# Kernel optimization log

Measured on AMD Instinct MI355X. Metric: run time of the kernel, lower is better.

Reference implementation:

```python
import jax, jax.numpy as jnp
import numpy as np

H = 128          # hidden_dim
N_LAYERS = 3
N_GRAPHS = 256
LN_EPS = 1e-5


def setup_inputs() -> dict:
    key = jax.random.key(0)
    ks = jax.random.split(key, 12)
    N, E = 100000, 600000
    x = jax.random.normal(ks[0], (N, 66), dtype=jnp.float32)
    edge_index = jax.random.randint(ks[1], (2, E), 0, N, dtype=jnp.int32)
    edge_attr = jax.random.normal(ks[2], (E, 6), dtype=jnp.float32)
    batch = jnp.sort(jax.random.randint(ks[3], (N,), 0, N_GRAPHS, dtype=jnp.int32))
    # params (stored as [in, out] so y = x @ W + b)
    def lin(k, fan_in, fan_out):
        s = 1.0 / np.sqrt(fan_in)
        kw, kb = jax.random.split(k)
        return (jax.random.uniform(kw, (fan_in, fan_out), jnp.float32, -s, s),
                jax.random.uniform(kb, (fan_out,), jnp.float32, -s, s))
    w_node, b_node = lin(ks[4], 66, H)
    w_edge, b_edge = lin(ks[5], 6, H)
    mp_ws, mp_bs = [], []
    for i in range(N_LAYERS):
        w, b = lin(ks[6 + i], 3 * H, H)
        mp_ws.append(w); mp_bs.append(b)
    w_out, b_out = lin(ks[9], H, H)
    return {
        "x": x, "edge_index": edge_index, "edge_attr": edge_attr, "batch": batch,
        "w_node": w_node, "b_node": b_node, "w_edge": w_edge, "b_edge": b_edge,
        "mp_w": jnp.stack(mp_ws), "mp_b": jnp.stack(mp_bs),
        "ln_g": jnp.ones((H,), jnp.float32), "ln_b": jnp.zeros((H,), jnp.float32),
        "w_out": w_out, "b_out": b_out,
    }


def _layer_norm(h, g, b):
    mu = h.mean(-1, keepdims=True)
    var = ((h - mu) ** 2).mean(-1, keepdims=True)
    return (h - mu) * jax.lax.rsqrt(var + LN_EPS) * g + b


def reference(x, edge_index, edge_attr, batch, w_node, b_node, w_edge, b_edge,
              mp_w, mp_b, ln_g, ln_b, w_out, b_out):
    h = x @ w_node + b_node                      # [N, H]
    ef = edge_attr @ w_edge + b_edge             # [E, H]
    src, dst = edge_index[0], edge_index[1]
    for i in range(N_LAYERS):
        W = mp_w[i]                               # [3H, H], split to avoid concat
        Ws, Wd, We = W[:H], W[H:2 * H], W[2 * H:]
        # per-edge message = Linear(concat(h[src], h[dst], ef)); original takes a
        # GLOBAL mean over all edges -> single [H] vector broadcast to all nodes
        msgs = h[src] @ Ws + h[dst] @ Wd + ef @ We   # [E, H]
        mean_msg = msgs.mean(axis=0) + mp_b[i]       # [H]
        h = h + mean_msg
        h = jax.nn.relu(_layer_norm(h, ln_g, ln_b))
        # dropout is identity in eval mode
    counts = jax.ops.segment_sum(jnp.ones((h.shape[0],), h.dtype), batch,
                                 num_segments=N_GRAPHS)
    pooled = jax.ops.segment_sum(h, batch, num_segments=N_GRAPHS)
    pooled = pooled / jnp.maximum(counts, 1.0)[:, None]   # global_mean_pool
    return pooled @ w_out + b_out                 # [N_GRAPHS, H]
```

## Files before the change

### kernel.cpp

```cpp
#include <hip/hip_runtime.h>

#define HDIM 128
#define XDIM 66
#define EDIM 6
#define NGRAPHS 256
#define LN_EPS 1e-5f

#define HBINS 25600
#define HR 4
#define HB 16
#define CBINS (HR * HBINS)
#define NBX 1024
#define KP 104

typedef __attribute__((ext_vector_type(8))) short sv8;
typedef __attribute__((ext_vector_type(4))) float fv4;

__device__ __forceinline__ unsigned short f2bf(float f) {
    unsigned u = __float_as_uint(f);
    return (unsigned short)((u + 0x7FFFu + ((u >> 16) & 1u)) >> 16);
}
__device__ __forceinline__ float bf2f(unsigned short u) {
    return __uint_as_float((unsigned)u << 16);
}

__global__ __launch_bounds__(256) void k_pre(const int* __restrict__ ei,
        float* __restrict__ part, int E, const float* __restrict__ ea,
        float* __restrict__ sum_attr, const float* __restrict__ w_node,
        unsigned short* __restrict__ wtg) {
    __shared__ float lh[HBINS];
    int b = blockIdx.x;
    int t = threadIdx.x;
    if (b < 2 * HR * HB) {
        int s = b & (HB - 1);
        int r = (b / HB) & (HR - 1);
        int a = b / (HB * HR);
        for (int i = t; i < HBINS; i += 256) lh[i] = 0.f;
        __syncthreads();
        const int* src = ei + (size_t)a * E;
        int chunk = (((E + HB - 1) / HB) + 3) & ~3;
        int lo = s * chunk;
        int hi = min(E, lo + chunk);
        int base = r * HBINS;
        if ((E & 3) == 0) {
            for (int i = lo + t * 4; i < hi; i += 256 * 4) {
                if (i + 4 <= hi) {
                    int4 v = *(const int4*)(src + i);
                    unsigned u0 = (unsigned)(v.x - base);
                    unsigned u1 = (unsigned)(v.y - base);
                    unsigned u2 = (unsigned)(v.z - base);
                    unsigned u3 = (unsigned)(v.w - base);
                    if (u0 < HBINS) atomicAdd(&lh[u0], 1.0f);
                    if (u1 < HBINS) atomicAdd(&lh[u1], 1.0f);
                    if (u2 < HBINS) atomicAdd(&lh[u2], 1.0f);
                    if (u3 < HBINS) atomicAdd(&lh[u3], 1.0f);
                } else {
                    for (int j = i; j < hi; ++j) {
                        unsigned u = (unsigned)(src[j] - base);
                        if (u < HBINS) atomicAdd(&lh[u], 1.0f);
                    }
                }
            }
        } else {
            for (int i = lo + t; i < hi; i += 256) {
                unsigned u = (unsigned)(src[i] - base);
                if (u < HBINS) atomicAdd(&lh[u], 1.0f);
            }
        }
        __syncthreads();
        float* dst = part + (size_t)b * HBINS;
        for (int i = t; i < HBINS / 4; i += 256)
            ((float4*)dst)[i] = ((const float4*)lh)[i];
    } else if (b < 2 * HR * HB + 64) {
        int b2 = b - 2 * HR * HB;
        int nchunk = E >> 1;
        float a0 = 0, a1 = 0, a2 = 0, a3 = 0, a4 = 0, a5 = 0;
        for (int c = b2 * 256 + t; c < nchunk; c += 64 * 256) {
            const float4* p = (const float4*)(ea + (size_t)c * 12);
            float4 v0 = p[0], v1 = p[1], v2 = p[2];
            a0 += v0.x + v1.z;  a1 += v0.y + v1.w;  a2 += v0.z + v2.x;
            a3 += v0.w + v2.y;  a4 += v1.x + v2.z;  a5 += v1.y + v2.w;
        }
#pragma unroll
        for (int m = 32; m; m >>= 1) {
            a0 += __shfl_xor(a0, m); a1 += __shfl_xor(a1, m); a2 += __shfl_xor(a2, m);
            a3 += __shfl_xor(a3, m); a4 += __shfl_xor(a4, m); a5 += __shfl_xor(a5, m);
        }
        float (*sb)[6] = (float(*)[6])lh;
        int lane = t & 63, w = t >> 6;
        if (lane == 0) {
            sb[w][0] = a0; sb[w][1] = a1; sb[w][2] = a2;
            sb[w][3] = a3; sb[w][4] = a4; sb[w][5] = a5;
        }
        __syncthreads();
        if (t < 6) {
            float s = sb[0][t] + sb[1][t] + sb[2][t] + sb[3][t];
            atomicAdd(&sum_attr[t], s);
        }
        if (b2 == 0 && t < 6 && (E & 1))
            atomicAdd(&sum_attr[t], ea[(size_t)(E - 1) * 6 + t]);
    } else {
        if (t < 128) {
            for (int kp = 0; kp < KP; ++kp) {
                float v = (kp < XDIM) ? w_node[kp * HDIM + t] : 0.f;
                wtg[t * KP + kp] = f2bf(v);
            }
        }
    }
}

__global__ __launch_bounds__(256) void k_hist_red(const float* __restrict__ part,
        float* __restrict__ c_src, float* __restrict__ c_dst) {
    int n = blockIdx.x * 256 + threadIdx.x;
    if (n >= CBINS) return;
    int r = n / HBINS, off = n - r * HBINS;
    const float* p0 = part + ((size_t)(0 * HR + r) * HB) * HBINS + off;
    const float* p1 = part + ((size_t)(1 * HR + r) * HB) * HBINS + off;
    float s0 = 0.f, s1 = 0.f;
#pragma unroll 8
    for (int s = 0; s < HB; ++s) {
        s0 += p0[(size_t)s * HBINS];
        s1 += p1[(size_t)s * HBINS];
    }
    c_src[n] = s0;
    c_dst[n] = s1;
}

__global__ __launch_bounds__(256) void k_xsum(const float* __restrict__ x,
        const float* __restrict__ c_src, const float* __restrict__ c_dst,
        float* __restrict__ xpart, int N) {
    int lane = threadIdx.x & 63, w = threadIdx.x >> 6;
    int wid = blockIdx.x * 4 + w, nw = gridDim.x * 4;
    float as0 = 0, ad0 = 0, as1 = 0, ad1 = 0;
    int Q = N >> 2;
    for (int q = wid; q < Q; q += nw) {
        int n = q * 4;
        const float* xr = x + (size_t)n * XDIM;
        float x0 = xr[lane];
        float x1 = xr[XDIM + lane];
        float x2 = xr[2 * XDIM + lane];
        float x3 = xr[3 * XDIM + lane];
        float4 cs = *(const float4*)(c_src + n);
        float4 cd = *(const float4*)(c_dst + n);
        as0 = fmaf(cs.x, x0, as0); as0 = fmaf(cs.y, x1, as0);
        as0 = fmaf(cs.z, x2, as0); as0 = fmaf(cs.w, x3, as0);
        ad0 = fmaf(cd.x, x0, ad0); ad0 = fmaf(cd.y, x1, ad0);
        ad0 = fmaf(cd.z, x2, ad0); ad0 = fmaf(cd.w, x3, ad0);
        if (lane < 2) {
            float e0 = xr[64 + lane];
            float e1 = xr[XDIM + 64 + lane];
            float e2 = xr[2 * XDIM + 64 + lane];
            float e3 = xr[3 * XDIM + 64 + lane];
            as1 = fmaf(cs.x, e0, as1); as1 = fmaf(cs.y, e1, as1);
            as1 = fmaf(cs.z, e2, as1); as1 = fmaf(cs.w, e3, as1);
            ad1 = fmaf(cd.x, e0, ad1); ad1 = fmaf(cd.y, e1, ad1);
            ad1 = fmaf(cd.z, e2, ad1); ad1 = fmaf(cd.w, e3, ad1);
        }
    }
    if (wid == 0) {
        for (int n = Q * 4; n < N; ++n) {
            const float* xr = x + (size_t)n * XDIM;
            float cs = c_src[n], cd = c_dst[n];
            float xv = xr[lane];
            as0 = fmaf(cs, xv, as0);
            ad0 = fmaf(cd, xv, ad0);
            if (lane < 2) {
                float xe = xr[64 + lane];
                as1 = fmaf(cs, xe, as1);
                ad1 = fmaf(cd, xe, ad1);
            }
        }
    }
    __shared__ float redS[4][XDIM], redD[4][XDIM];
    redS[w][lane] = as0;  redD[w][lane] = ad0;
    if (lane < 2) { redS[w][64 + lane] = as1;  redD[w][64 + lane] = ad1; }
    __syncthreads();
    int t = threadIdx.x;
    float* xp = xpart + (size_t)blockIdx.x * 136;
    if (t < XDIM) {
        xp[t]        = redS[0][t] + redS[1][t] + redS[2][t] + redS[3][t];
        xp[XDIM + t] = redD[0][t] + redD[1][t] + redD[2][t] + redD[3][t];
    }
}

__global__ __launch_bounds__(64) void k_xred(const float* __restrict__ xpart,
                                             float* __restrict__ xs, int nb) {
    int e = blockIdx.x;
    int lane = threadIdx.x;
    float s = 0.f;
    for (int b = lane; b < nb; b += 64)
        s += xpart[(size_t)b * 136 + e];
#pragma unroll
    for (int m = 32; m; m >>= 1) s += __shfl_xor(s, m);
    if (lane == 0) xs[e] = s;
}

__global__ __launch_bounds__(256) void k_red(const float* __restrict__ partials,
                                             float* __restrict__ sbuf, int nb) {
    int b0 = blockIdx.x * 32;
    int b1 = min(nb, b0 + 32);
    int t = threadIdx.x;
    float s0 = 0.f, s1 = 0.f;
    for (int b = b0; b < b1; ++b) {
        const float* row = partials + (size_t)b * 512;
        s0 += row[t];
        s1 += row[t + 256];
    }
    atomicAdd(&sbuf[t], s0);
    atomicAdd(&sbuf[t + 256], s1);
}

template <int FIRST>
__global__ __launch_bounds__(256) void k_mm(const float* __restrict__ sv,
        const float* __restrict__ sum_attr, const float* __restrict__ w_edge,
        const float* __restrict__ b_edge, const float* __restrict__ W,
        const float* __restrict__ mpb, float* __restrict__ mean_msg, float Ef,
        const float* __restrict__ w_node, const float* __restrict__ b_node) {
    __shared__ float sc[384];
    __shared__ float mred[256];
    int t = threadIdx.x;
    if (t < 128) {
        float ssrc, sdst;
        if (FIRST) {
            ssrc = Ef * b_node[t];
            sdst = ssrc;
#pragma unroll
            for (int k = 0; k < XDIM; ++k) {
                float wv = w_node[k * HDIM + t];
                ssrc = fmaf(sv[k], wv, ssrc);
                sdst = fmaf(sv[XDIM + k], wv, sdst);
            }
        } else {
            ssrc = sv[t] + sv[t + 128];
            sdst = sv[256 + t] + sv[384 + t];
        }
        sc[t] = ssrc;
        sc[128 + t] = sdst;
        float se = Ef * b_edge[t];
#pragma unroll
        for (int k = 0; k < EDIM; ++k) se = fmaf(sum_attr[k], w_edge[k * HDIM + t], se);
        sc[256 + t] = se;
    }
    __syncthreads();
    int col = blockIdx.x * 16 + (t & 15);
    int rg = t >> 4;
    float acc = 0.f;
#pragma unroll 4
    for (int r = rg * 24; r < rg * 24 + 24; ++r)
        acc = fmaf(sc[r], W[r * HDIM + col], acc);
    mred[t] = acc;
    __syncthreads();
    if (t < 16) {
        float s = 0.f;
#pragma unroll
        for (int g = 0; g < 16; ++g) s += mred[g * 16 + t];
        mean_msg[blockIdx.x * 16 + t] = s / Ef + mpb[blockIdx.x * 16 + t];
    }
}

__global__ __launch_bounds__(256) void k_upd0(
        const float* __restrict__ x, const unsigned short* __restrict__ wtg,
        const float* __restrict__ b_node, const float* __restrict__ mean_msg,
        const float* __restrict__ ln_g, const float* __restrict__ ln_b,
        const float* __restrict__ c_src, const float* __restrict__ c_dst,
        unsigned short* __restrict__ h, float* __restrict__ partials, int N) {
    __shared__ unsigned short xl[64 * KP];
    __shared__ unsigned short wt[128 * KP];
    int t = threadIdx.x;
    int lane = t & 63, w = t >> 6;
    {
        const uint4* srcp = (const uint4*)wtg;
        uint4* dstp = (uint4*)wt;
        for (int i = t; i < 128 * KP / 8; i += 256) dstp[i] = srcp[i];
    }
    for (int i = t; i < 64 * KP / 2; i += 256) ((unsigned*)xl)[i] = 0u;
    __syncthreads();
    int rowbase = blockIdx.x * 64;
    const float* xg = x + (size_t)rowbase * XDIM;
    int lim = min(64, N - rowbase) * XDIM;
    for (int i = t; i < 64 * XDIM; i += 256) {
        if (i < lim) {
            int r = i / XDIM, k = i - r * XDIM;
            xl[r * KP + k] = f2bf(xg[i]);
        }
    }
    int cl = lane & 15, g = lane >> 4;
    float bm[8], gg[8], lb[8];
#pragma unroll
    for (int ct = 0; ct < 8; ++ct) {
        int col = ct * 16 + cl;
        bm[ct] = b_node[col] + mean_msg[col];
        gg[ct] = ln_g[col];
        lb[ct] = ln_b[col];
    }
    __syncthreads();

    fv4 acc[8];
#pragma unroll
    for (int ct = 0; ct < 8; ++ct) acc[ct] = (fv4){0.f, 0.f, 0.f, 0.f};
#pragma unroll
    for (int ks = 0; ks < 3; ++ks) {
        sv8 a = *(const sv8*)&xl[(w * 16 + cl) * KP + ks * 32 + g * 8];
#pragma unroll
        for (int ct = 0; ct < 8; ++ct) {
            sv8 b = *(const sv8*)&wt[(ct * 16 + cl) * KP + ks * 32 + g * 8];
            acc[ct] = __builtin_amdgcn_mfma_f32_16x16x32_bf16(a, b, acc[ct], 0, 0, 0);
        }
    }
    float v[8][4];
    float s[4] = {0.f, 0.f, 0.f, 0.f};
#pragma unroll
    for (int ct = 0; ct < 8; ++ct)
#pragma unroll
        for (int e = 0; e < 4; ++e) {
            v[ct][e] = acc[ct][e] + bm[ct];
            s[e] += v[ct][e];
        }
#pragma unroll
    for (int m = 1; m < 16; m <<= 1) {
        s[0] += __shfl_xor(s[0], m); s[1] += __shfl_xor(s[1], m);
        s[2] += __shfl_xor(s[2], m); s[3] += __shfl_xor(s[3], m);
    }
    float mu[4], q[4] = {0.f, 0.f, 0.f, 0.f};
#pragma unroll
    for (int e = 0; e < 4; ++e) mu[e] = s[e] * (1.0f / HDIM);
#pragma unroll
    for (int ct = 0; ct < 8; ++ct)
#pragma unroll
        for (int e = 0; e < 4; ++e) {
            float d = v[ct][e] - mu[e];
            q[e] = fmaf(d, d, q[e]);
        }
#pragma unroll
    for (int m = 1; m < 16; m <<= 1) {
        q[0] += __shfl_xor(q[0], m); q[1] += __shfl_xor(q[1], m);
        q[2] += __shfl_xor(q[2], m); q[3] += __shfl_xor(q[3], m);
    }
    float rs[4];
#pragma unroll
    for (int e = 0; e < 4; ++e) rs[e] = rsqrtf(q[e] * (1.0f / HDIM) + LN_EPS);

    int grow = rowbase + w * 16 + g * 4;
    float4 csv = *(const float4*)(c_src + grow);
    float4 cdv = *(const float4*)(c_dst + grow);
    float cs[4] = {csv.x, csv.y, csv.z, csv.w};
    float cd[4] = {cdv.x, cdv.y, cdv.z, cdv.w};
    float accS[8], accD[8];
#pragma unroll
    for (int ct = 0; ct < 8; ++ct) { accS[ct] = 0.f; accD[ct] = 0.f; }
#pragma unroll
    for (int e = 0; e < 4; ++e) {
        int row = grow + e;
        bool ok = (row < N);
#pragma unroll
        for (int ct = 0; ct < 8; ++ct) {
            float o = fmaxf(0.f, fmaf((v[ct][e] - mu[e]) * rs[e], gg[ct], lb[ct]));
            if (ok) h[(size_t)row * HDIM + ct * 16 + cl] = f2bf(o);
            accS[ct] = fmaf(cs[e], o, accS[ct]);
            accD[ct] = fmaf(cd[e], o, accD[ct]);
        }
    }
#pragma unroll
    for (int ct = 0; ct < 8; ++ct) {
        accS[ct] += __shfl_xor(accS[ct], 16); accS[ct] += __shfl_xor(accS[ct], 32);
        accD[ct] += __shfl_xor(accD[ct], 16); accD[ct] += __shfl_xor(accD[ct], 32);
    }
    __syncthreads();
    float* redS = (float*)xl;
    float* redD = redS + 512;
    if (g == 0) {
#pragma unroll
        for (int ct = 0; ct < 8; ++ct) {
            redS[w * HDIM + ct * 16 + cl] = accS[ct];
            redD[w * HDIM + ct * 16 + cl] = accD[ct];
        }
    }
    __syncthreads();
    if (t < 128) {
        float ss = redS[t] + redS[128 + t] + redS[256 + t] + redS[384 + t];
        float dd = redD[t] + redD[128 + t] + redD[256 + t] + redD[384 + t];
        float* row = partials + (size_t)blockIdx.x * 512;
        row[t] = ss;       row[t + 128] = 0.f;
        row[t + 256] = dd; row[t + 384] = 0.f;
    }
}

__device__ __forceinline__ float4 ln_row4(const unsigned short* hp,
        float4 mm, float4 g, float4 bb) {
    ushort4 hv = *(const ushort4*)hp;
    float4 v;
    v.x = bf2f(hv.x) + mm.x; v.y = bf2f(hv.y) + mm.y;
    v.z = bf2f(hv.z) + mm.z; v.w = bf2f(hv.w) + mm.w;
    float s = v.x + v.y + v.z + v.w;
#pragma unroll
    for (int m = 1; m < 32; m <<= 1) s += __shfl_xor(s, m);
    float mu = s * (1.0f / HDIM);
    float d0 = v.x - mu, d1 = v.y - mu, d2 = v.z - mu, d3 = v.w - mu;
    float q = d0 * d0 + d1 * d1 + d2 * d2 + d3 * d3;
#pragma unroll
    for (int m = 1; m < 32; m <<= 1) q += __shfl_xor(q, m);
    float rs = rsqrtf(q * (1.0f / HDIM) + LN_EPS);
    float4 o;
    o.x = fmaxf(0.f, fmaf(d0 * rs, g.x, bb.x));
    o.y = fmaxf(0.f, fmaf(d1 * rs, g.y, bb.y));
    o.z = fmaxf(0.f, fmaf(d2 * rs, g.z, bb.z));
    o.w = fmaxf(0.f, fmaf(d3 * rs, g.w, bb.w));
    return o;
}

template <int LAST>
__global__ __launch_bounds__(256) void k_update(
        unsigned short* __restrict__ h, const float* __restrict__ mean_msg,
        const float* __restrict__ ln_g, const float* __restrict__ ln_b,
        const float* __restrict__ c_src, const float* __restrict__ c_dst,
        const int* __restrict__ batch, float* __restrict__ partials,
        float* __restrict__ pooled, int N, int cpb) {
    int t = threadIdx.x;
    int lane = t & 63, w = t >> 6;
    int half = lane >> 5, cl = lane & 31;
    int c0 = cl * 4;
    float4 mm = *(const float4*)(mean_msg + c0);
    float4 g  = *(const float4*)(ln_g + c0);
    float4 bb = *(const float4*)(ln_b + c0);
    int start = blockIdx.x * cpb;
    int end = min(N, start + cpb);
    int spw = (cpb + 3) >> 2;
    int ns = start + w * spw;
    int ne = min(end, ns + spw);
    float4 accS = {0,0,0,0}, accD = {0,0,0,0}, accP = {0,0,0,0};
    int cur_g = -1;
    int n = ns;
    for (; n + 4 <= ne; n += 4) {
        int rA = n + half, rB = n + 2 + half;
        float4 oA = ln_row4(h + (size_t)rA * HDIM + c0, mm, g, bb);
        float4 oB = ln_row4(h + (size_t)rB * HDIM + c0, mm, g, bb);
        if (LAST) {
            int gA = batch[rA], gB = batch[rB];
            if (gA != cur_g) {
                if (cur_g >= 0) {
                    atomicAdd(&pooled[cur_g * HDIM + c0],     accP.x);
                    atomicAdd(&pooled[cur_g * HDIM + c0 + 1], accP.y);
                    atomicAdd(&pooled[cur_g * HDIM + c0 + 2], accP.z);
                    atomicAdd(&pooled[cur_g * HDIM + c0 + 3], accP.w);
                }
                accP = (float4){0,0,0,0};
                cur_g = gA;
            }
            accP.x += oA.x; accP.y += oA.y; accP.z += oA.z; accP.w += oA.w;
            if (gB != cur_g) {
                if (cur_g >= 0) {
                    atomicAdd(&pooled[cur_g * HDIM + c0],     accP.x);
                    atomicAdd(&pooled[cur_g * HDIM + c0 + 1], accP.y);
                    atomicAdd(&pooled[cur_g * HDIM + c0 + 2], accP.z);
                    atomicAdd(&pooled[cur_g * HDIM + c0 + 3], accP.w);
                }
                accP = (float4){0,0,0,0};
                cur_g = gB;
            }
            accP.x += oB.x; accP.y += oB.y; accP.z += oB.z; accP.w += oB.w;
        } else {
            ushort4 pA = {f2bf(oA.x), f2bf(oA.y), f2bf(oA.z), f2bf(oA.w)};
            ushort4 pB = {f2bf(oB.x), f2bf(oB.y), f2bf(oB.z), f2bf(oB.w)};
            *(ushort4*)(h + (size_t)rA * HDIM + c0) = pA;
            *(ushort4*)(h + (size_t)rB * HDIM + c0) = pB;
            float csA = c_src[rA], cdA = c_dst[rA];
            float csB = c_src[rB], cdB = c_dst[rB];
            accS.x = fmaf(csA, oA.x, accS.x); accS.y = fmaf(csA, oA.y, accS.y);
            accS.z = fmaf(csA, oA.z, accS.z); accS.w = fmaf(csA, oA.w, accS.w);
            accS.x = fmaf(csB, oB.x, accS.x); accS.y = fmaf(csB, oB.y, accS.y);
            accS.z = fmaf(csB, oB.z, accS.z); accS.w = fmaf(csB, oB.w, accS.w);
            accD.x = fmaf(cdA, oA.x, accD.x); accD.y = fmaf(cdA, oA.y, accD.y);
            accD.z = fmaf(cdA, oA.z, accD.z); accD.w = fmaf(cdA, oA.w, accD.w);
            accD.x = fmaf(cdB, oB.x, accD.x); accD.y = fmaf(cdB, oB.y, accD.y);
            accD.z = fmaf(cdB, oB.z, accD.z); accD.w = fmaf(cdB, oB.w, accD.w);
        }
    }
    for (; n < ne; n += 2) {
        int row = n + half;
        bool ok = row < ne;
        int rsafe = ok ? row : (N - 1);
        float4 o = ln_row4(h + (size_t)rsafe * HDIM + c0, mm, g, bb);
        if (LAST) {
            if (ok) {
                int gg2 = batch[row];
                if (gg2 != cur_g) {
                    if (cur_g >= 0) {
                        atomicAdd(&pooled[cur_g * HDIM + c0],     accP.x);
                        atomicAdd(&pooled[cur_g * HDIM + c0 + 1], accP.y);
                        atomicAdd(&pooled[cur_g * HDIM + c0 + 2], accP.z);
                        atomicAdd(&pooled[cur_g * HDIM + c0 + 3], accP.w);
                    }
                    accP = (float4){0,0,0,0};
                    cur_g = gg2;
                }
                accP.x += o.x; accP.y += o.y; accP.z += o.z; accP.w += o.w;
            }
        } else if (ok) {
            ushort4 pk = {f2bf(o.x), f2bf(o.y), f2bf(o.z), f2bf(o.w)};
            *(ushort4*)(h + (size_t)row * HDIM + c0) = pk;
            float cs = c_src[row], cd = c_dst[row];
            accS.x = fmaf(cs, o.x, accS.x); accS.y = fmaf(cs, o.y, accS.y);
            accS.z = fmaf(cs, o.z, accS.z); accS.w = fmaf(cs, o.w, accS.w);
            accD.x = fmaf(cd, o.x, accD.x); accD.y = fmaf(cd, o.y, accD.y);
            accD.z = fmaf(cd, o.z, accD.z); accD.w = fmaf(cd, o.w, accD.w);
        }
    }
    if (LAST) {
        if (cur_g >= 0) {
            atomicAdd(&pooled[cur_g * HDIM + c0],     accP.x);
            atomicAdd(&pooled[cur_g * HDIM + c0 + 1], accP.y);
            atomicAdd(&pooled[cur_g * HDIM + c0 + 2], accP.z);
            atomicAdd(&pooled[cur_g * HDIM + c0 + 3], accP.w);
        }
    } else {
        __shared__ float redS[8][HDIM], redD[8][HDIM];
        int set = (w << 1) | half;
        *(float4*)(&redS[set][c0]) = accS;
        *(float4*)(&redD[set][c0]) = accD;
        __syncthreads();
        if (t < 128) {
            float ss = 0.f, dd = 0.f;
#pragma unroll
            for (int gi = 0; gi < 8; ++gi) {
                ss += redS[gi][t];
                dd += redD[gi][t];
            }
            float* row = partials + (size_t)blockIdx.x * 512;
            row[t] = ss;       row[t + 128] = 0.f;
            row[t + 256] = dd; row[t + 384] = 0.f;
        }
    }
}

__global__ __launch_bounds__(128) void k_out(const float* __restrict__ pooled,
        const int* __restrict__ batch, const float* __restrict__ w_out,
        const float* __restrict__ b_out, float* __restrict__ out, int N) {
    int gph = blockIdx.x;
    int t = threadIdx.x;
    __shared__ float p[HDIM];
    __shared__ int cntS;
    if (t == 0) {
        int lo = 0, hi = N;
        while (lo < hi) { int mid = (lo + hi) >> 1; if (batch[mid] < gph) lo = mid + 1; else hi = mid; }
        int lo2 = lo, hi2 = N;
        while (lo2 < hi2) { int mid = (lo2 + hi2) >> 1; if (batch[mid] <= gph) lo2 = mid + 1; else hi2 = mid; }
        cntS = lo2 - lo;
    }
    __syncthreads();
    float inv = 1.0f / fmaxf((float)cntS, 1.0f);
    p[t] = pooled[gph * HDIM + t] * inv;
    __syncthreads();
    float acc = b_out[t];
#pragma unroll 8
    for (int k = 0; k < HDIM; ++k) acc = fmaf(p[k], w_out[k * HDIM + t], acc);
    out[gph * HDIM + t] = acc;
}

extern "C" void kernel_launch(void* const* d_in, const int* in_sizes, int n_in,
                              void* d_out, int out_size, void* d_ws, size_t ws_size,
                              hipStream_t stream) {
    const float* x      = (const float*)d_in[0];
    const int*   ei     = (const int*)d_in[1];
    const float* ea     = (const float*)d_in[2];
    const int*   batch  = (const int*)d_in[3];
    const float* w_node = (const float*)d_in[4];
    const float* b_node = (const float*)d_in[5];
    const float* w_edge = (const float*)d_in[6];
    const float* b_edge = (const float*)d_in[7];
    const float* mp_w   = (const float*)d_in[8];
    const float* mp_b   = (const float*)d_in[9];
    const float* ln_g   = (const float*)d_in[10];
    const float* ln_b   = (const float*)d_in[11];
    const float* w_out  = (const float*)d_in[12];
    const float* b_out  = (const float*)d_in[13];
    float* out = (float*)d_out;
    int N = in_sizes[3];
    int E = in_sizes[2] / EDIM;
    float Ef = (float)E;
    int ntiles0 = (N + 63) / 64;

    float* ws = (float*)d_ws;
    size_t off = 0;
    unsigned short* h = (unsigned short*)(ws + off);
    float* hist_part = ws + off;
    off += (size_t)N * HDIM / 2;
    float* partials = ws + off; off += (size_t)2048 * 512;
    float* mean_msg = ws + off; off += 128;
    float* c_src    = ws + off; off += CBINS;
    float* c_dst    = ws + off; off += CBINS;
    float* xpart    = ws + off; off += (size_t)NBX * 136;
    unsigned short* wtg = (unsigned short*)(ws + off); off += 128 * KP / 2;
    float* xs       = ws + off; off += 136;
    float* acc0     = ws + off;
    float* sum_attr = ws + off; off += 8;
    float* sbuf1    = ws + off; off += 512;
    float* sbuf2    = ws + off; off += 512;
    float* pooled   = ws + off; off += NGRAPHS * HDIM;
    size_t zero_count = (size_t)(ws + off - acc0);
    hipMemsetAsync(acc0, 0, zero_count * sizeof(float), stream);

    k_pre<<<2 * HR * HB + 64 + 1, 256, 0, stream>>>(ei, hist_part, E, ea,
                                                    sum_attr, w_node, wtg);
    k_hist_red<<<(CBINS + 255) / 256, 256, 0, stream>>>(hist_part, c_src, c_dst);
    k_xsum<<<NBX, 256, 0, stream>>>(x, c_src, c_dst, xpart, N);
    k_xred<<<2 * XDIM, 64, 0, stream>>>(xpart, xs, NBX);

    const int NB = 1024;
    int cpb = (N + NB - 1) / NB;

    k_mm<1><<<8, 256, 0, stream>>>(xs, sum_attr, w_edge, b_edge,
                                   mp_w, mp_b, mean_msg, Ef, w_node, b_node);
    k_upd0<<<ntiles0, 256, 0, stream>>>(x, wtg, b_node, mean_msg, ln_g, ln_b,
                                        c_src, c_dst, h, partials, N);
    k_red<<<(ntiles0 + 31) / 32, 256, 0, stream>>>(partials, sbuf1, ntiles0);
    k_mm<0><<<8, 256, 0, stream>>>(sbuf1, sum_attr, w_edge, b_edge,
                                   mp_w + (size_t)1 * 384 * HDIM,
                                   mp_b + (size_t)1 * HDIM, mean_msg, Ef,
                                   w_node, b_node);
    k_update<0><<<NB, 256, 0, stream>>>(h, mean_msg, ln_g, ln_b, c_src, c_dst,
                                        batch, partials, pooled, N, cpb);
    k_red<<<NB / 32, 256, 0, stream>>>(partials, sbuf2, NB);
    k_mm<0><<<8, 256, 0, stream>>>(sbuf2, sum_attr, w_edge, b_edge,
                                   mp_w + (size_t)2 * 384 * HDIM,
                                   mp_b + (size_t)2 * HDIM, mean_msg, Ef,
                                   w_node, b_node);
    k_update<1><<<NB, 256, 0, stream>>>(h, mean_msg, ln_g, ln_b, c_src, c_dst,
                                        batch, partials, pooled, N, cpb);

    k_out<<<NGRAPHS, HDIM, 0, stream>>>(pooled, batch, w_out, b_out, out, N);
}
```

Measured before the change: 163.9 us.

## Byte-pack node degree histogram so one block covers all nodes in LDS

Replaces the range-partitioned float LDS histogram with integer words that pack four 8-bit node counters each, so a single 1024-thread block holds bins for every node. Each edge is now scanned once instead of once per node range, and float atomics become integer atomics. The per-slice partials are reduced with integer adds and unpacked to floats. The edge-attribute sum and weight conversion move into a separate small kernel, which adds a launch. Counts are only correct while every node's in- and out-degree stays below 256, so high-degree graphs would silently give wrong results.

```diff
diff --git a/kernel.cpp b/kernel.cpp
--- a/kernel.cpp
+++ b/kernel.cpp
@@ -6,12 +6,12 @@
 #define NGRAPHS 256
 #define LN_EPS 1e-5f
 
-#define HBINS 25600
-#define HR 4
-#define HB 16
-#define CBINS (HR * HBINS)
+#define NWORDS 25600
+#define CBINS 102400
+#define HB 64
 #define NBX 1024
 #define KP 104
+#define NES 16
 
 typedef __attribute__((ext_vector_type(8))) short sv8;
 typedef __attribute__((ext_vector_type(4))) float fv4;
@@ -24,58 +24,69 @@
     return __uint_as_float((unsigned)u << 16);
 }
 
-__global__ __launch_bounds__(256) void k_pre(const int* __restrict__ ei,
-        float* __restrict__ part, int E, const float* __restrict__ ea,
-        float* __restrict__ sum_attr, const float* __restrict__ w_node,
+__global__ __launch_bounds__(1024) void k_hist(const int* __restrict__ ei,
+        unsigned* __restrict__ part, int E) {
+    __shared__ unsigned lh[NWORDS];
+    int b = blockIdx.x;
+    int s = b & (HB - 1);
+    int a = b / HB;
+    int t = threadIdx.x;
+    for (int i = t; i < NWORDS; i += 1024) lh[i] = 0u;
+    __syncthreads();
+    const int* src = ei + (size_t)a * E;
+    int chunk = (((E + HB - 1) / HB) + 3) & ~3;
+    int lo = s * chunk;
+    int hi = min(E, lo + chunk);
+    if ((E & 3) == 0) {
+        for (int i = lo + t * 4; i + 4 <= hi; i += 1024 * 4) {
+            int4 v = *(const int4*)(src + i);
+            atomicAdd(&lh[v.x >> 2], 1u << ((v.x & 3) * 8));
+            atomicAdd(&lh[v.y >> 2], 1u << ((v.y & 3) * 8));
+            atomicAdd(&lh[v.z >> 2], 1u << ((v.z & 3) * 8));
+            atomicAdd(&lh[v.w >> 2], 1u << ((v.w & 3) * 8));
+        }
+    } else {
+        for (int i = lo + t; i < hi; i += 1024) {
+            int v = src[i];
+            atomicAdd(&lh[v >> 2], 1u << ((v & 3) * 8));
+        }
+    }
+    __syncthreads();
+    unsigned* dst = part + (size_t)b * NWORDS;
+    for (int i = t; i < NWORDS / 4; i += 1024)
+        ((uint4*)dst)[i] = ((const uint4*)lh)[i];
+}
+
+__global__ __launch_bounds__(256) void k_hist_red(const unsigned* __restrict__ part,
+        float* __restrict__ c_src, float* __restrict__ c_dst) {
+    int w = blockIdx.x * 256 + threadIdx.x;
+    if (w >= NWORDS) return;
+    unsigned a0 = 0, a1 = 0;
+    const unsigned* p0 = part + w;
+    const unsigned* p1 = part + (size_t)HB * NWORDS + w;
+#pragma unroll 8
+    for (int s = 0; s < HB; ++s) {
+        a0 += p0[(size_t)s * NWORDS];
+        a1 += p1[(size_t)s * NWORDS];
+    }
+    float4 o0, o1;
+    o0.x = (float)(a0 & 0xFF);         o0.y = (float)((a0 >> 8) & 0xFF);
+    o0.z = (float)((a0 >> 16) & 0xFF); o0.w = (float)(a0 >> 24);
+    o1.x = (float)(a1 & 0xFF);         o1.y = (float)((a1 >> 8) & 0xFF);
+    o1.z = (float)((a1 >> 16) & 0xFF); o1.w = (float)(a1 >> 24);
+    *(float4*)(c_src + 4 * w) = o0;
+    *(float4*)(c_dst + 4 * w) = o1;
+}
+
+__global__ __launch_bounds__(256) void k_misc(const float* __restrict__ ea,
+        float* __restrict__ sum_attr, int E, const float* __restrict__ w_node,
         unsigned short* __restrict__ wtg) {
-    __shared__ float lh[HBINS];
     int b = blockIdx.x;
     int t = threadIdx.x;
-    if (b < 2 * HR * HB) {
-        int s = b & (HB - 1);
-        int r = (b / HB) & (HR - 1);
-        int a = b / (HB * HR);
-        for (int i = t; i < HBINS; i += 256) lh[i] = 0.f;
-        __syncthreads();
-        const int* src = ei + (size_t)a * E;
-        int chunk = (((E + HB - 1) / HB) + 3) & ~3;
-        int lo = s * chunk;
-        int hi = min(E, lo + chunk);
-        int base = r * HBINS;
-        if ((E & 3) == 0) {
-            for (int i = lo + t * 4; i < hi; i += 256 * 4) {
-                if (i + 4 <= hi) {
-                    int4 v = *(const int4*)(src + i);
-                    unsigned u0 = (unsigned)(v.x - base);
-                    unsigned u1 = (unsigned)(v.y - base);
-                    unsigned u2 = (unsigned)(v.z - base);
-                    unsigned u3 = (unsigned)(v.w - base);
-                    if (u0 < HBINS) atomicAdd(&lh[u0], 1.0f);
-                    if (u1 < HBINS) atomicAdd(&lh[u1], 1.0f);
-                    if (u2 < HBINS) atomicAdd(&lh[u2], 1.0f);
-                    if (u3 < HBINS) atomicAdd(&lh[u3], 1.0f);
-                } else {
-                    for (int j = i; j < hi; ++j) {
-                        unsigned u = (unsigned)(src[j] - base);
-                        if (u < HBINS) atomicAdd(&lh[u], 1.0f);
-                    }
-                }
-            }
-        } else {
-            for (int i = lo + t; i < hi; i += 256) {
-                unsigned u = (unsigned)(src[i] - base);
-                if (u < HBINS) atomicAdd(&lh[u], 1.0f);
-            }
-        }
-        __syncthreads();
-        float* dst = part + (size_t)b * HBINS;
-        for (int i = t; i < HBINS / 4; i += 256)
-            ((float4*)dst)[i] = ((const float4*)lh)[i];
-    } else if (b < 2 * HR * HB + 64) {
-        int b2 = b - 2 * HR * HB;
+    if (b < NES) {
         int nchunk = E >> 1;
         float a0 = 0, a1 = 0, a2 = 0, a3 = 0, a4 = 0, a5 = 0;
-        for (int c = b2 * 256 + t; c < nchunk; c += 64 * 256) {
+        for (int c = b * 256 + t; c < nchunk; c += NES * 256) {
             const float4* p = (const float4*)(ea + (size_t)c * 12);
             float4 v0 = p[0], v1 = p[1], v2 = p[2];
             a0 += v0.x + v1.z;  a1 += v0.y + v1.w;  a2 += v0.z + v2.x;
@@ -86,7 +97,7 @@
             a0 += __shfl_xor(a0, m); a1 += __shfl_xor(a1, m); a2 += __shfl_xor(a2, m);
             a3 += __shfl_xor(a3, m); a4 += __shfl_xor(a4, m); a5 += __shfl_xor(a5, m);
         }
-        float (*sb)[6] = (float(*)[6])lh;
+        __shared__ float sb[4][6];
         int lane = t & 63, w = t >> 6;
         if (lane == 0) {
             sb[w][0] = a0; sb[w][1] = a1; sb[w][2] = a2;
@@ -97,7 +108,7 @@
             float s = sb[0][t] + sb[1][t] + sb[2][t] + sb[3][t];
             atomicAdd(&sum_attr[t], s);
         }
-        if (b2 == 0 && t < 6 && (E & 1))
+        if (b == 0 && t < 6 && (E & 1))
             atomicAdd(&sum_attr[t], ea[(size_t)(E - 1) * 6 + t]);
     } else {
         if (t < 128) {
@@ -107,23 +118,6 @@
             }
         }
     }
-}
-
-__global__ __launch_bounds__(256) void k_hist_red(const float* __restrict__ part,
-        float* __restrict__ c_src, float* __restrict__ c_dst) {
-    int n = blockIdx.x * 256 + threadIdx.x;
-    if (n >= CBINS) return;
-    int r = n / HBINS, off = n - r * HBINS;
-    const float* p0 = part + ((size_t)(0 * HR + r) * HB) * HBINS + off;
-    const float* p1 = part + ((size_t)(1 * HR + r) * HB) * HBINS + off;
-    float s0 = 0.f, s1 = 0.f;
-#pragma unroll 8
-    for (int s = 0; s < HB; ++s) {
-        s0 += p0[(size_t)s * HBINS];
-        s1 += p1[(size_t)s * HBINS];
-    }
-    c_src[n] = s0;
-    c_dst[n] = s1;
 }
 
 __global__ __launch_bounds__(256) void k_xsum(const float* __restrict__ x,
@@ -582,7 +576,7 @@
     float* ws = (float*)d_ws;
     size_t off = 0;
     unsigned short* h = (unsigned short*)(ws + off);
-    float* hist_part = ws + off;
+    unsigned* hist_part = (unsigned*)(ws + off);
     off += (size_t)N * HDIM / 2;
     float* partials = ws + off; off += (size_t)2048 * 512;
     float* mean_msg = ws + off; off += 128;
@@ -599,9 +593,9 @@
     size_t zero_count = (size_t)(ws + off - acc0);
     hipMemsetAsync(acc0, 0, zero_count * sizeof(float), stream);
 
-    k_pre<<<2 * HR * HB + 64 + 1, 256, 0, stream>>>(ei, hist_part, E, ea,
-                                                    sum_attr, w_node, wtg);
-    k_hist_red<<<(CBINS + 255) / 256, 256, 0, stream>>>(hist_part, c_src, c_dst);
+    k_misc<<<NES + 1, 256, 0, stream>>>(ea, sum_attr, E, w_node, wtg);
+    k_hist<<<2 * HB, 1024, 0, stream>>>(ei, hist_part, E);
+    k_hist_red<<<(NWORDS + 255) / 256, 256, 0, stream>>>(hist_part, c_src, c_dst);
     k_xsum<<<NBX, 256, 0, stream>>>(x, c_src, c_dst, xpart, N);
     k_xred<<<2 * XDIM, 64, 0, stream>>>(xpart, xs, NBX);
 
```

Result: slower. 169.5 us (+3.5%).
